# Kernel optimization log

Hardware: AMD Instinct MI355X
Metric: run time of the kernel (lower is better)

Reference implementation:

```python
import jax, jax.numpy as jnp
import numpy as np

BS, SEQ, IN, H, L = 32, 2048, 512, 256, 2


def _cell(x_t, h, W1, b1, W2, b2):
    # blending1(x, x, x): gate1*x + (1-gate1)*x  (kept literal for faithfulness)
    g1 = jax.nn.sigmoid(x_t @ W1.T + b1)
    left = g1 * x_t + (1.0 - g1) * x_t
    # blending2(h, x, x): gate from x, blend h and x
    g2 = jax.nn.sigmoid(x_t @ W2.T + b2)
    right = g2 * h + (1.0 - g2) * x_t
    return jnp.tanh(left * right)


def _run_dir(x_seq, h0, W1, b1, W2, b2):
    # x_seq: [seq, bs, H]; sequential recurrence via scan
    def step(h, x_t):
        h_new = _cell(x_t, h, W1, b1, W2, b2)
        return h_new, h_new
    h_last, ys = jax.lax.scan(step, h0, x_seq)
    return ys, h_last  # ys: [seq, bs, H], h_last: [bs, H]


def setup_inputs() -> dict:
    key = jax.random.key(0)
    ks = jax.random.split(key, 7)
    std = 1.0 / np.sqrt(H)
    return {
        "x": jax.random.normal(ks[0], (BS, SEQ, IN), dtype=jnp.float32),
        "W_fc": jax.random.uniform(ks[1], (H, IN), jnp.float32, -std, std),
        "b_fc": jax.random.uniform(ks[2], (H,), jnp.float32, -std, std),
        "W1": jax.random.uniform(ks[3], (L, H, H), jnp.float32, -std, std),
        "b1": jax.random.uniform(ks[4], (L, H), jnp.float32, -std, std),
        "W2": jax.random.uniform(ks[5], (L, H, H), jnp.float32, -std, std),
        "b2": jax.random.uniform(ks[6], (L, H), jnp.float32, -std, std),
    }


def reference(x, W_fc, b_fc, W1, b1, W2, b2):
    bs, seq, _ = x.shape
    Hh = W_fc.shape[0]
    n_layers = W1.shape[0]
    # input projection, then duplicate along features: [bs, seq, 2H]
    h = x @ W_fc.T + b_fc
    xx = jnp.concatenate([h, h], axis=2)
    h_finals = []
    for i in range(n_layers):
        # split halves: left-to-right on first half, right-to-left on flipped second half
        ltr = jnp.swapaxes(xx[:, :, :Hh], 0, 1)                      # [seq, bs, H]
        rtl = jnp.swapaxes(jnp.flip(xx[:, :, Hh:], axis=1), 0, 1)    # [seq, bs, H]
        h0 = jnp.zeros((bs, Hh), dtype=xx.dtype)
        y_l, h_l = _run_dir(ltr, h0, W1[i], b1[i], W2[i], b2[i])
        y_r, h_r = _run_dir(rtl, h0, W1[i], b1[i], W2[i], b2[i])
        y_l = jnp.swapaxes(y_l, 0, 1)                                # [bs, seq, H]
        y_r = jnp.flip(jnp.swapaxes(y_r, 0, 1), axis=1)
        xx = jnp.concatenate([y_l, y_r], axis=2)                     # [bs, seq, 2H]
        h_finals.append(jnp.stack([h_l, h_r], axis=0))               # [2, bs, H]
    h_out = jnp.concatenate(h_finals, axis=0)                        # [2L, bs, H]
    return xx, h_out
```

## Files before the change

### kernel.cpp

```cpp
#include <hip/hip_runtime.h>

#define SEQL 2048
#define BSZ  32
#define HDIM 256
#define MTOT (BSZ*SEQL)
#define XXN  ((size_t)MTOT*512)

typedef short v8s __attribute__((ext_vector_type(8)));
typedef float v4f __attribute__((ext_vector_type(4)));

__device__ __forceinline__ short f2bf(float f) {
  return __builtin_bit_cast(short, (__bf16)f);
}

__device__ __forceinline__ v8s pack8(float4 a, float4 b) {
  v8s r;
  r[0] = f2bf(a.x); r[1] = f2bf(a.y); r[2] = f2bf(a.z); r[3] = f2bf(a.w);
  r[4] = f2bf(b.x); r[5] = f2bf(b.y); r[6] = f2bf(b.z); r[7] = f2bf(b.w);
  return r;
}

__global__ __launch_bounds__(256, 3) void gemm_bias_act(
    const float* __restrict__ A, int sa,
    const float* __restrict__ W, int K,
    const float* __restrict__ bias,
    float* __restrict__ C, int act)
{
  __shared__ short As[2][128*40];
  __shared__ short Bs[2][128*40];

  int tid  = threadIdx.x;
  int m0   = blockIdx.x * 128;
  int n0   = blockIdx.y * 128;
  int lane = tid & 63;
  int wid  = tid >> 6;
  int wr   = wid >> 1, wc = wid & 1;
  int quad = lane >> 4, r16 = lane & 15;

  int srow = tid >> 1;
  int sseg = (tid & 1) * 16;

  v4f acc[4][4];
  #pragma unroll
  for (int i = 0; i < 4; ++i)
    #pragma unroll
    for (int j = 0; j < 4; ++j)
      acc[i][j] = (v4f){0.f, 0.f, 0.f, 0.f};

  const float* aB = A + (long)(m0 + srow)*sa + sseg;
  const float* wB = W + (long)(n0 + srow)*K + sseg;

  float4 aCur[4], bCur[4];
  #pragma unroll
  for (int u = 0; u < 4; ++u) {
    aCur[u] = ((const float4*)aB)[u];
    bCur[u] = ((const float4*)wB)[u];
  }

  for (int kk = 0; kk < K; kk += 32) {
    short* Asb = As[(kk >> 5) & 1];
    short* Bsb = Bs[(kk >> 5) & 1];

    *(v8s*)&Asb[srow*40 + sseg]     = pack8(aCur[0], aCur[1]);
    *(v8s*)&Asb[srow*40 + sseg + 8] = pack8(aCur[2], aCur[3]);
    *(v8s*)&Bsb[srow*40 + sseg]     = pack8(bCur[0], bCur[1]);
    *(v8s*)&Bsb[srow*40 + sseg + 8] = pack8(bCur[2], bCur[3]);
    __syncthreads();

    if (kk + 32 < K) {
      const float4* ap = (const float4*)(aB + kk + 32);
      const float4* wp = (const float4*)(wB + kk + 32);
      #pragma unroll
      for (int u = 0; u < 4; ++u) { aCur[u] = ap[u]; bCur[u] = wp[u]; }
    }

    v8s af[4], bfv[4];
    #pragma unroll
    for (int i = 0; i < 4; ++i)
      af[i] = *(const v8s*)&Asb[(wr*64 + i*16 + r16)*40 + quad*8];
    #pragma unroll
    for (int j = 0; j < 4; ++j)
      bfv[j] = *(const v8s*)&Bsb[(wc*64 + j*16 + r16)*40 + quad*8];
    #pragma unroll
    for (int i = 0; i < 4; ++i)
      #pragma unroll
      for (int j = 0; j < 4; ++j)
        acc[i][j] = __builtin_amdgcn_mfma_f32_16x16x32_bf16(af[i], bfv[j], acc[i][j], 0, 0, 0);
  }

  #pragma unroll
  for (int j = 0; j < 4; ++j) {
    int col = n0 + wc*64 + j*16 + r16;
    float bv = bias[col];
    #pragma unroll
    for (int i = 0; i < 4; ++i) {
      int rowb = m0 + wr*64 + i*16 + quad*4;
      #pragma unroll
      for (int r = 0; r < 4; ++r) {
        float v = acc[i][j][r] + bv;
        if (act) {
          float e = __builtin_amdgcn_exp2f(v * -1.4426950408889634f);
          v = __builtin_amdgcn_rcpf(1.f + e);
        }
        C[(long)(rowb + r)*HDIM + col] = v;
      }
    }
  }
}

__global__ __launch_bounds__(64) void recur(
    const float* __restrict__ X, int sx, int xoffR,
    const float* __restrict__ G, int sg, int goffR,
    float* __restrict__ Y, float* __restrict__ hout)
{
  const int T = 16;
  const int SEGS = 8;
  const int SEGLEN = SEQL / SEGS;
  const int WARM = 64;

  int blk = blockIdx.x & 255;
  int seg = blockIdx.x >> 8;
  int fg = blk & 3;
  int b  = (blk >> 2) & 31;
  int d  = blk >> 7;
  int f  = fg*64 + threadIdx.x;

  int u0    = seg*SEGLEN - (seg ? WARM : 0);
  int warmc = seg ? (WARM/T) : 0;
  int nc    = warmc + SEGLEN/T;
  int half  = nc >> 1;

  int stp  = d ? -1 : 1;
  int t0   = d ? (SEQL-1 - u0) : u0;
  int xoff = d ? xoffR : 0;
  int goff = d ? goffR : 0;

  const float* xc = X + (long)(b*SEQL + t0)*sx + xoff + f;
  const float* gc = G + (long)(b*SEQL + t0)*sg + goff + f;
  long xstep = (long)stp * sx;
  long gstep = (long)stp * sg;

  int ty0 = d ? (SEQL-1 - seg*SEGLEN) : seg*SEGLEN;
  float* yp = Y + (long)(b*SEQL + ty0)*512 + d*HDIM + f;
  long ystep = (long)stp * 512;

  const float K   = 2.8853900817779268f;
  const float mK2 = -5.7707801635558537f;

  float Ax[T], Ag[T], Bx[T], Bg[T], hb[T];
  #pragma unroll
  for (int j = 0; j < T; ++j) { Ax[j] = xc[xstep*j]; Ag[j] = gc[gstep*j]; }

  float r = 0.5f;

  auto compute = [&](float* xb, float* gb) {
    #pragma unroll
    for (int j = 0; j < T; ++j) {
      float x = xb[j], g = gb[j];
      float a = x * g;
      float m = a * mK2;
      float n = K * fmaf(x, x - a, a);
      float q = fmaf(m, r, n);
      float E = __builtin_amdgcn_exp2f(q);
      r = __builtin_amdgcn_rcpf(E + 1.0f);
      hb[j] = fmaf(-2.0f, r, 1.0f);
    }
  };
  auto flush = [&](int c) {
    if (c >= warmc) {
      #pragma unroll
      for (int j = 0; j < T; ++j) yp[ystep*j] = hb[j];
      yp += ystep*T;
    }
  };

  int c = 0;
  for (int it = 0; it < half; ++it) {
    const float* xn = xc + xstep*T;
    const float* gn = gc + gstep*T;
    #pragma unroll
    for (int j = 0; j < T; ++j) { Bx[j] = xn[xstep*j]; Bg[j] = gn[gstep*j]; }
    compute(Ax, Ag); flush(c);
    bool hv = (c+2 < nc);
    const float* xn2 = hv ? xn + xstep*T : xn;
    const float* gn2 = hv ? gn + gstep*T : gn;
    #pragma unroll
    for (int j = 0; j < T; ++j) { Ax[j] = xn2[xstep*j]; Ag[j] = gn2[gstep*j]; }
    compute(Bx, Bg); flush(c+1);
    xc = xn2; gc = gn2; c += 2;
  }

  if (seg == SEGS-1)
    hout[(size_t)d*BSZ*HDIM + (size_t)b*HDIM + f] = fmaf(-2.0f, r, 1.0f);
}

extern "C" void kernel_launch(void* const* d_in, const int* in_sizes, int n_in,
                              void* d_out, int out_size, void* d_ws, size_t ws_size,
                              hipStream_t stream) {
  const float* x    = (const float*)d_in[0];
  const float* W_fc = (const float*)d_in[1];
  const float* b_fc = (const float*)d_in[2];
  const float* W2   = (const float*)d_in[5];
  const float* b2   = (const float*)d_in[6];

  float* out  = (float*)d_out;
  float* bufA = (float*)d_ws;
  float* bufB = bufA + (size_t)MTOT*HDIM;
  float* xx   = out;
  float* hout = out + XXN;

  gemm_bias_act<<<dim3(512,2), 256, 0, stream>>>(x, 512, W_fc, 512, b_fc, bufA, 0);
  gemm_bias_act<<<dim3(512,2), 256, 0, stream>>>(bufA, HDIM, W2, HDIM, b2, bufB, 1);
  recur<<<2048, 64, 0, stream>>>(bufA, HDIM, 0, bufB, HDIM, 0, xx, hout);
  gemm_bias_act<<<dim3(1024,2), 256, 0, stream>>>(xx, HDIM, W2 + HDIM*HDIM, HDIM, b2 + HDIM, bufA, 1);
  recur<<<2048, 64, 0, stream>>>(xx, 512, 256, bufA, 512, 256, xx, hout + 2*BSZ*HDIM);
}
```

Measured before the change: 519.5 us.

## Use 8 waves per GEMM block with single-barrier double-buffered prefetch

```diff
diff --git a/kernel.cpp b/kernel.cpp
--- a/kernel.cpp
+++ b/kernel.cpp
@@ -20,7 +20,7 @@
   return r;
 }
 
-__global__ __launch_bounds__(256, 3) void gemm_bias_act(
+__global__ __launch_bounds__(512, 4) void gemm_bias_act(
     const float* __restrict__ A, int sa,
     const float* __restrict__ W, int K,
     const float* __restrict__ bias,
@@ -34,63 +34,72 @@
   int n0   = blockIdx.y * 128;
   int lane = tid & 63;
   int wid  = tid >> 6;
-  int wr   = wid >> 1, wc = wid & 1;
+  int wr   = wid >> 2;
+  int wc   = wid & 3;
   int quad = lane >> 4, r16 = lane & 15;
 
-  int srow = tid >> 1;
-  int sseg = (tid & 1) * 16;
-
-  v4f acc[4][4];
+  int srow = tid >> 2;
+  int sq   = tid & 3;
+
+  v4f acc[4][2];
   #pragma unroll
   for (int i = 0; i < 4; ++i)
     #pragma unroll
-    for (int j = 0; j < 4; ++j)
+    for (int j = 0; j < 2; ++j)
       acc[i][j] = (v4f){0.f, 0.f, 0.f, 0.f};
 
-  const float* aB = A + (long)(m0 + srow)*sa + sseg;
-  const float* wB = W + (long)(n0 + srow)*K + sseg;
-
-  float4 aCur[4], bCur[4];
-  #pragma unroll
-  for (int u = 0; u < 4; ++u) {
-    aCur[u] = ((const float4*)aB)[u];
-    bCur[u] = ((const float4*)wB)[u];
-  }
-
-  for (int kk = 0; kk < K; kk += 32) {
-    short* Asb = As[(kk >> 5) & 1];
-    short* Bsb = Bs[(kk >> 5) & 1];
-
-    *(v8s*)&Asb[srow*40 + sseg]     = pack8(aCur[0], aCur[1]);
-    *(v8s*)&Asb[srow*40 + sseg + 8] = pack8(aCur[2], aCur[3]);
-    *(v8s*)&Bsb[srow*40 + sseg]     = pack8(bCur[0], bCur[1]);
-    *(v8s*)&Bsb[srow*40 + sseg + 8] = pack8(bCur[2], bCur[3]);
-    __syncthreads();
-
-    if (kk + 32 < K) {
-      const float4* ap = (const float4*)(aB + kk + 32);
-      const float4* wp = (const float4*)(wB + kk + 32);
-      #pragma unroll
-      for (int u = 0; u < 4; ++u) { aCur[u] = ap[u]; bCur[u] = wp[u]; }
-    }
-
-    v8s af[4], bfv[4];
+  const float* aB = A + (long)(m0 + srow)*sa + sq*8;
+  const float* wB = W + (long)(n0 + srow)*K + sq*8;
+
+  float4 a0x = ((const float4*)aB)[0],      a0y = ((const float4*)aB)[1];
+  float4 b0x = ((const float4*)wB)[0],      b0y = ((const float4*)wB)[1];
+  float4 a1x = ((const float4*)(aB+32))[0], a1y = ((const float4*)(aB+32))[1];
+  float4 b1x = ((const float4*)(wB+32))[0], b1y = ((const float4*)(wB+32))[1];
+
+  auto compute = [&](const short* Asb, const short* Bsb) {
+    v8s af[4], bfv[2];
     #pragma unroll
     for (int i = 0; i < 4; ++i)
       af[i] = *(const v8s*)&Asb[(wr*64 + i*16 + r16)*40 + quad*8];
     #pragma unroll
-    for (int j = 0; j < 4; ++j)
-      bfv[j] = *(const v8s*)&Bsb[(wc*64 + j*16 + r16)*40 + quad*8];
+    for (int j = 0; j < 2; ++j)
+      bfv[j] = *(const v8s*)&Bsb[(wc*32 + j*16 + r16)*40 + quad*8];
     #pragma unroll
     for (int i = 0; i < 4; ++i)
       #pragma unroll
-      for (int j = 0; j < 4; ++j)
+      for (int j = 0; j < 2; ++j)
         acc[i][j] = __builtin_amdgcn_mfma_f32_16x16x32_bf16(af[i], bfv[j], acc[i][j], 0, 0, 0);
+  };
+
+  for (int kk = 0; kk < K; kk += 64) {
+    *(v8s*)&As[0][srow*40 + sq*8] = pack8(a0x, a0y);
+    *(v8s*)&Bs[0][srow*40 + sq*8] = pack8(b0x, b0y);
+    asm volatile("s_waitcnt lgkmcnt(0)" ::: "memory");
+    __builtin_amdgcn_s_barrier();
+    {
+      int nk = (kk + 64 < K) ? kk + 64 : 0;
+      const float4* ap = (const float4*)(aB + nk);
+      const float4* wp = (const float4*)(wB + nk);
+      a0x = ap[0]; a0y = ap[1]; b0x = wp[0]; b0y = wp[1];
+    }
+    compute(As[0], Bs[0]);
+
+    *(v8s*)&As[1][srow*40 + sq*8] = pack8(a1x, a1y);
+    *(v8s*)&Bs[1][srow*40 + sq*8] = pack8(b1x, b1y);
+    asm volatile("s_waitcnt lgkmcnt(0)" ::: "memory");
+    __builtin_amdgcn_s_barrier();
+    {
+      int nk = (kk + 96 < K) ? kk + 96 : 32;
+      const float4* ap = (const float4*)(aB + nk);
+      const float4* wp = (const float4*)(wB + nk);
+      a1x = ap[0]; a1y = ap[1]; b1x = wp[0]; b1y = wp[1];
+    }
+    compute(As[1], Bs[1]);
   }
 
   #pragma unroll
-  for (int j = 0; j < 4; ++j) {
-    int col = n0 + wc*64 + j*16 + r16;
+  for (int j = 0; j < 2; ++j) {
+    int col = n0 + wc*32 + j*16 + r16;
     float bv = bias[col];
     #pragma unroll
     for (int i = 0; i < 4; ++i) {
@@ -209,9 +218,9 @@
   float* xx   = out;
   float* hout = out + XXN;
 
-  gemm_bias_act<<<dim3(512,2), 256, 0, stream>>>(x, 512, W_fc, 512, b_fc, bufA, 0);
-  gemm_bias_act<<<dim3(512,2), 256, 0, stream>>>(bufA, HDIM, W2, HDIM, b2, bufB, 1);
+  gemm_bias_act<<<dim3(512,2), 512, 0, stream>>>(x, 512, W_fc, 512, b_fc, bufA, 0);
+  gemm_bias_act<<<dim3(512,2), 512, 0, stream>>>(bufA, HDIM, W2, HDIM, b2, bufB, 1);
   recur<<<2048, 64, 0, stream>>>(bufA, HDIM, 0, bufB, HDIM, 0, xx, hout);
-  gemm_bias_act<<<dim3(1024,2), 256, 0, stream>>>(xx, HDIM, W2 + HDIM*HDIM, HDIM, b2 + HDIM, bufA, 1);
+  gemm_bias_act<<<dim3(1024,2), 512, 0, stream>>>(xx, HDIM, W2 + HDIM*HDIM, HDIM, b2 + HDIM, bufA, 1);
   recur<<<2048, 64, 0, stream>>>(xx, 512, 256, bufA, 512, 256, xx, hout + 2*BSZ*HDIM);
 }
```

New measurement: 667.9 us. 1.29x slower.

## Stage GEMM tiles via direct global-to-LDS loads with XOR swizzle

Applied to the files above, without the earlier changes.

```diff
diff --git a/kernel.cpp b/kernel.cpp
--- a/kernel.cpp
+++ b/kernel.cpp
@@ -8,37 +8,71 @@
 
 typedef short v8s __attribute__((ext_vector_type(8)));
 typedef float v4f __attribute__((ext_vector_type(4)));
+typedef const __attribute__((address_space(1))) void* gptr_t;
+typedef __attribute__((address_space(3))) void* sptr_t;
 
 __device__ __forceinline__ short f2bf(float f) {
   return __builtin_bit_cast(short, (__bf16)f);
 }
 
-__device__ __forceinline__ v8s pack8(float4 a, float4 b) {
-  v8s r;
-  r[0] = f2bf(a.x); r[1] = f2bf(a.y); r[2] = f2bf(a.z); r[3] = f2bf(a.w);
-  r[4] = f2bf(b.x); r[5] = f2bf(b.y); r[6] = f2bf(b.z); r[7] = f2bf(b.w);
-  return r;
-}
-
-__global__ __launch_bounds__(256, 3) void gemm_bias_act(
+__device__ __forceinline__ void gload16(const float* g, float* l) {
+  __builtin_amdgcn_global_load_lds((gptr_t)g, (sptr_t)l, 16, 0, 0);
+}
+
+__global__ __launch_bounds__(256) void gemm_bias_act(
     const float* __restrict__ A, int sa,
     const float* __restrict__ W, int K,
     const float* __restrict__ bias,
     float* __restrict__ C, int act)
 {
-  __shared__ short As[2][128*40];
-  __shared__ short Bs[2][128*40];
+  __shared__ float lds[16384];
 
   int tid  = threadIdx.x;
   int m0   = blockIdx.x * 128;
   int n0   = blockIdx.y * 128;
   int lane = tid & 63;
-  int wid  = tid >> 6;
-  int wr   = wid >> 1, wc = wid & 1;
+  int w    = tid >> 6;
+  int wr   = w >> 1, wc = w & 1;
   int quad = lane >> 4, r16 = lane & 15;
 
-  int srow = tid >> 1;
-  int sseg = (tid & 1) * 16;
+  int lrow = lane >> 3;
+  int js   = (lane & 7) ^ lrow;
+  const float* aSrc = A + (long)(m0 + w*8 + lrow)*sa + js*4;
+  const float* wSrc = W + (long)(n0 + w*8 + lrow)*K  + js*4;
+  float* ldsA = lds + w*256;
+  float* ldsB = lds + 4096 + w*256;
+
+  auto stage = [&](int buf, int kk) {
+    const float* a = aSrc + kk;
+    const float* b = wSrc + kk;
+    float* la = ldsA + buf*8192;
+    float* lb = ldsB + buf*8192;
+    #pragma unroll
+    for (int i = 0; i < 4; ++i) {
+      gload16(a + (long)i*32*sa, la + i*1024);
+      gload16(b + (long)i*32*K,  lb + i*1024);
+    }
+  };
+
+  int aoff[4][2], boff[4][2];
+  #pragma unroll
+  for (int i = 0; i < 4; ++i) {
+    int ra = wr*64 + i*16 + r16, sA = ra & 7;
+    aoff[i][0] = ra*32 + ((2*quad)     ^ sA)*4;
+    aoff[i][1] = ra*32 + ((2*quad + 1) ^ sA)*4;
+    int rb = wc*64 + i*16 + r16, sB = rb & 7;
+    boff[i][0] = rb*32 + ((2*quad)     ^ sB)*4;
+    boff[i][1] = rb*32 + ((2*quad + 1) ^ sB)*4;
+  }
+
+  auto loadfrag = [&](const float* base, const int* o) {
+    float4 f0 = *(const float4*)(base + o[0]);
+    float4 f1 = *(const float4*)(base + o[1]);
+    v8s r;
+    r[0] = f2bf(f0.x); r[1] = f2bf(f0.y); r[2] = f2bf(f0.z); r[3] = f2bf(f0.w);
+    r[4] = f2bf(f1.x); r[5] = f2bf(f1.y); r[6] = f2bf(f1.z); r[7] = f2bf(f1.w);
+    return r;
+  };
 
   v4f acc[4][4];
   #pragma unroll
@@ -47,40 +81,18 @@
     for (int j = 0; j < 4; ++j)
       acc[i][j] = (v4f){0.f, 0.f, 0.f, 0.f};
 
-  const float* aB = A + (long)(m0 + srow)*sa + sseg;
-  const float* wB = W + (long)(n0 + srow)*K + sseg;
-
-  float4 aCur[4], bCur[4];
-  #pragma unroll
-  for (int u = 0; u < 4; ++u) {
-    aCur[u] = ((const float4*)aB)[u];
-    bCur[u] = ((const float4*)wB)[u];
-  }
-
-  for (int kk = 0; kk < K; kk += 32) {
-    short* Asb = As[(kk >> 5) & 1];
-    short* Bsb = Bs[(kk >> 5) & 1];
-
-    *(v8s*)&Asb[srow*40 + sseg]     = pack8(aCur[0], aCur[1]);
-    *(v8s*)&Asb[srow*40 + sseg + 8] = pack8(aCur[2], aCur[3]);
-    *(v8s*)&Bsb[srow*40 + sseg]     = pack8(bCur[0], bCur[1]);
-    *(v8s*)&Bsb[srow*40 + sseg + 8] = pack8(bCur[2], bCur[3]);
+  stage(0, 0);
+  int nt = K >> 5;
+  for (int t = 0; t < nt; ++t) {
     __syncthreads();
-
-    if (kk + 32 < K) {
-      const float4* ap = (const float4*)(aB + kk + 32);
-      const float4* wp = (const float4*)(wB + kk + 32);
-      #pragma unroll
-      for (int u = 0; u < 4; ++u) { aCur[u] = ap[u]; bCur[u] = wp[u]; }
-    }
-
+    if (t + 1 < nt) stage((t + 1) & 1, (t + 1) * 32);
+    const float* Ab = lds + (t & 1)*8192;
+    const float* Bb = Ab + 4096;
     v8s af[4], bfv[4];
     #pragma unroll
-    for (int i = 0; i < 4; ++i)
-      af[i] = *(const v8s*)&Asb[(wr*64 + i*16 + r16)*40 + quad*8];
-    #pragma unroll
-    for (int j = 0; j < 4; ++j)
-      bfv[j] = *(const v8s*)&Bsb[(wc*64 + j*16 + r16)*40 + quad*8];
+    for (int i = 0; i < 4; ++i) af[i]  = loadfrag(Ab, aoff[i]);
+    #pragma unroll
+    for (int j = 0; j < 4; ++j) bfv[j] = loadfrag(Bb, boff[j]);
     #pragma unroll
     for (int i = 0; i < 4; ++i)
       #pragma unroll
```

Measured after the change: 524.9 us. No clear change (+1.0%).
